# Optimization experiments

Measured on AMD Instinct MI355X. Metric: run time of the kernel, lower is better.

Reference implementation:

```python
import jax, jax.numpy as jnp
import numpy as np

B, P, G, E = 2, 16, 128, 96
C110, C011, C001 = 4, 2, 1
N, CO = 128, 2

def _pw(x, W, b):
    """1x1 conv of any spatial rank == pointwise channel mixing."""
    y = jnp.einsum('oc,bc...->bo...', W, x)
    return y + b.reshape((1, -1) + (1,) * (y.ndim - 2))

def _hidden(s110, s011, s001, Ws, bs):
    # s110:[B,C,P,G,1]  s011:[B,C,1,G,E]  s001:[B,C,1,1,E]
    # sub-stream order: [110 full, 110 pool-P, 110 pool-G, 011 full, 011 pool-G, 011 pool-E, 001]
    t110 = s110[..., 0]         # [B,C,P,G]
    t011 = s011[:, :, 0]        # [B,C,G,E]
    t001 = s001[:, :, 0, 0]     # [B,C,E]
    s = (_pw(t110, Ws[0], bs[0])[..., None]
         + _pw(t110.max(axis=2), Ws[1], bs[1])[:, :, None, :, None]
         + _pw(t110.max(axis=3), Ws[2], bs[2])[:, :, :, None, None]
         + _pw(t011, Ws[3], bs[3])[:, :, None, :, :]
         + _pw(t011.max(axis=2), Ws[4], bs[4])[:, :, None, None, :]
         + _pw(t011.max(axis=3), Ws[5], bs[5])[:, :, None, :, None]
         + _pw(t001, Ws[6], bs[6])[:, :, None, None, :])
    s = jax.nn.leaky_relu(s)    # [B,N,P,G,E]
    return (jnp.max(s, axis=4, keepdims=True),
            jnp.max(s, axis=2, keepdims=True),
            jnp.max(s, axis=(2, 3), keepdims=True))

def _forward(x110, x011, x001, W0_110, b0_110, W0_011, b0_011, W0_001, b0_001, W1, b1, Wact, bact, Wcrit, bcrit):
    Ws0 = [W0_110[0], W0_110[1], W0_110[2], W0_011[0], W0_011[1], W0_011[2], W0_001]
    bs0 = [b0_110[0], b0_110[1], b0_110[2], b0_011[0], b0_011[1], b0_011[2], b0_001]
    s110, s011, s001 = _hidden(x110, x011, x001, Ws0, bs0)
    s110, s011, s001 = _hidden(s110, s011, s001, list(W1), list(b1))
    t110 = s110[..., 0]  # [B,N,P,G]
    # actor head: eliminate G,E via mean pooling (dim_elimination_max_pooling=False)
    a110 = _pw(t110.mean(axis=3), Wact[0], bact[0])              # [B,CO,P]
    a011 = _pw(s011.mean(axis=(3, 4)), Wact[1], bact[1])         # [B,CO,1]
    a001 = _pw(s001[:, :, :, 0].mean(axis=3), Wact[2], bact[2])  # [B,CO,1]
    actions = jax.nn.leaky_relu(a110 + a011 + a001)              # [B,CO,P]
    # critic head: eliminate G via mean pooling
    c110 = _pw(t110.mean(axis=3), Wcrit[0], bcrit[0])            # [B,CO,P]
    c011 = _pw(s011[:, :, 0].mean(axis=2), Wcrit[1], bcrit[1])   # [B,CO,E]
    c001 = _pw(s001[:, :, 0, 0], Wcrit[2], bcrit[2])             # [B,CO,E]
    v = jax.nn.leaky_relu(c110[:, :, :, None] + (c011 + c001)[:, :, None, :])  # [B,CO,P,E]
    v110 = v.max(axis=3).sum(axis=2)  # stream (1,1,0): max over E, sum over P
    v011 = v.max(axis=2).sum(axis=2)  # streams (0,1,1) and (0,0,1) coincide numerically
    values = (2.0 + v110 + 2.0 * v011).reshape(-1)  # python sum(l, 2) starts at 2
    return actions, values

def setup_inputs() -> dict:
    key = jax.random.key(0)
    ks = jax.random.split(key, 12)
    f32 = jnp.float32
    def w(k, shape, fan):
        return jax.random.normal(k, shape, f32) / np.float32(np.sqrt(fan))
    return {
        'x110': jax.random.normal(ks[0], (B, C110, P, G, 1), f32),
        'x011': jax.random.normal(ks[1], (B, C011, 1, G, E), f32),
        'x001': jax.random.normal(ks[2], (B, C001, 1, 1, E), f32),
        'W0_110': w(ks[3], (3, N, C110), C110), 'b0_110': jnp.zeros((3, N), f32),
        'W0_011': w(ks[4], (3, N, C011), C011), 'b0_011': jnp.zeros((3, N), f32),
        'W0_001': w(ks[5], (N, C001), C001),    'b0_001': jnp.zeros((N,), f32),
        'W1':     w(ks[6], (7, N, N), N),       'b1':     jnp.zeros((7, N), f32),
        'Wact':   w(ks[7], (3, CO, N), N),      'bact':   jnp.zeros((3, CO), f32),
        'Wcrit':  w(ks[8], (3, CO, N), N),      'bcrit':  jnp.zeros((3, CO), f32),
    }

def reference(x110, x011, x001, W0_110, b0_110, W0_011, b0_011, W0_001, b0_001, W1, b1, Wact, bact, Wcrit, bcrit):
    return _forward(x110, x011, x001, W0_110, b0_110, W0_011, b0_011, W0_001, b0_001, W1, b1, Wact, bact, Wcrit, bcrit)
```

## Files before the change

kernel.cpp:

```cpp
#include <hip/hip_runtime.h>
#include <math.h>

#define DEVI __device__ __forceinline__

constexpr int B = 2, P = 16, G = 128, E = 96, N = 128, CO = 2;

DEVI float lrelu(float x) { return x > 0.f ? x : 0.01f * x; }

constexpr int OFF_U1     = 0;
constexpr int OFF_V1     = OFF_U1 + 524288;
constexpr int OFF_MAXPU0 = OFF_V1 + 3145728;
constexpr int OFF_MAXEV0 = OFF_MAXPU0 + 32768;
constexpr int OFF_MP110  = OFF_MAXEV0 + 32768;
constexpr int OFF_MG110  = OFF_MP110 + 32768;
constexpr int OFF_S001A  = OFF_MG110 + 4096;
constexpr int OFF_RMP    = OFF_S001A + 24576;
constexpr int OFF_RMG    = OFF_RMP + 1024;
constexpr int OFF_RME    = OFF_RMG + 128;
constexpr int OFF_RMG011 = OFF_RME + 512;
constexpr int OFF_M110   = OFF_RMG011 + 384;
constexpr int OFF_M011E  = OFF_M110 + 4096;
constexpr int OFF_S001B  = OFF_M011E + 24576;
constexpr int OFF_WT     = OFF_S001B + 24576;
constexpr int OFF_PART   = OFF_WT + 81920;

__global__ void __launch_bounds__(256) k_layer0(
    const float* __restrict__ x110, const float* __restrict__ x011,
    const float* __restrict__ x001,
    const float* __restrict__ W0_110, const float* __restrict__ b0_110,
    const float* __restrict__ W0_011, const float* __restrict__ b0_011,
    const float* __restrict__ W0_001, const float* __restrict__ b0_001,
    const float* __restrict__ W1,
    float* __restrict__ maxpU0g, float* __restrict__ maxeV0g,
    float* __restrict__ mp110, float* __restrict__ mg110,
    float* __restrict__ s001a,
    float* __restrict__ rmpG, float* __restrict__ rmgG,
    float* __restrict__ rmeG, float* __restrict__ rmg011G,
    float* __restrict__ wT) {
  __shared__ float xs[4 * 16 * 128];
  __shared__ float v0[128 * 97];
  __shared__ float u0[16 * 128];
  __shared__ float rmp[512], rmgS[64], rme[256], rmg011L[192];
  __shared__ float mpu[128], mev[128], part[256];
  const int bn = blockIdx.x, b = bn >> 7, n = bn & 127, tid = threadIdx.x;

  {
    const float4* xsrc = (const float4*)(x110 + (size_t)b * 8192);
    float4* xdst = (float4*)xs;
#pragma unroll
    for (int k = 0; k < 8; k++) xdst[tid + k * 256] = xsrc[tid + k * 256];
  }
  __syncthreads();
  for (int i = tid; i < 512; i += 256) {
    int c = i >> 7, g = i & 127;
    float m = -INFINITY;
    for (int p = 0; p < P; p++) m = fmaxf(m, xs[(c * 16 + p) * 128 + g]);
    rmp[i] = m;
  }
  if (tid < 64) {
    int c = tid >> 4, p = tid & 15;
    float m = -INFINITY;
    for (int g = 0; g < G; g++) m = fmaxf(m, xs[(c * 16 + p) * 128 + g]);
    rmgS[tid] = m;
  }
  {
    int c = tid >> 7, g = tid & 127;
    const float4* r = (const float4*)(x011 + ((size_t)(b * 2 + c) * 128 + g) * 96);
    float m = -INFINITY;
#pragma unroll
    for (int j = 0; j < 24; j++) {
      float4 v = r[j];
      m = fmaxf(m, fmaxf(fmaxf(v.x, v.y), fmaxf(v.z, v.w)));
    }
    rme[tid] = m;
  }
  if (tid < 192) {
    int c = tid / 96, e = tid % 96;
    const float* pp = x011 + ((size_t)(b * 2 + c) * 128) * 96 + e;
    float m = -INFINITY;
    for (int g = 0; g < G; g++) m = fmaxf(m, pp[g * 96]);
    rmg011L[tid] = m;
  }
  __syncthreads();
  float w0[4], w1[4], w2[4];
#pragma unroll
  for (int cc = 0; cc < 4; cc++) {
    w0[cc] = W0_110[n * 4 + cc];
    w1[cc] = W0_110[512 + n * 4 + cc];
    w2[cc] = W0_110[1024 + n * 4 + cc];
  }
  float we0 = W0_011[512 + n * 2], we1 = W0_011[512 + n * 2 + 1];
  float bu = b0_110[n] + b0_110[128 + n] + b0_110[256 + n] + b0_011[256 + n];
  float vw00 = W0_011[n * 2], vw01 = W0_011[n * 2 + 1];
  float vw10 = W0_011[256 + n * 2], vw11 = W0_011[256 + n * 2 + 1];
  float w001 = W0_001[n];
  float bv = b0_011[n] + b0_011[128 + n] + b0_001[n];

#pragma unroll
  for (int k = 0; k < 8; k++) {
    int i = tid + k * 256, p = i >> 7, g = i & 127;
    float acc = bu + we0 * rme[g] + we1 * rme[128 + g];
#pragma unroll
    for (int cc = 0; cc < 4; cc++)
      acc += w0[cc] * xs[(cc * 16 + p) * 128 + g] + w1[cc] * rmp[cc * 128 + g]
           + w2[cc] * rmgS[cc * 16 + p];
    u0[i] = acc;
  }
  {
    const float* xa = x011 + (size_t)(b * 2) * 12288;
    const float* xb = xa + 12288;
    const float* xc = x001 + b * 96;
    for (int k = 0; k < 48; k++) {
      int i = tid + k * 256;
      int g = i / 96, e = i - g * 96;
      float val = bv + vw00 * xa[i] + vw01 * xb[i]
                + vw10 * rmg011L[e] + vw11 * rmg011L[96 + e] + w001 * xc[e];
      v0[g * 97 + e] = val;
    }
  }
  __syncthreads();
  if (tid < 128) {
    float m = -INFINITY;
    for (int p = 0; p < P; p++) m = fmaxf(m, u0[p * 128 + tid]);
    mpu[tid] = m;
    maxpU0g[bn * 128 + tid] = m;
  }
  {
    int g = tid & 127, h = tid >> 7;
    const float* r = &v0[g * 97 + h * 48];
    float m = -INFINITY;
    for (int j = 0; j < 48; j++) m = fmaxf(m, r[j]);
    part[tid] = m;
  }
  __syncthreads();
  if (tid < 128) {
    float m = fmaxf(part[tid], part[128 + tid]);
    mev[tid] = m;
    maxeV0g[bn * 128 + tid] = m;
    mp110[bn * 128 + tid] = lrelu(mpu[tid] + m);
  }
  __syncthreads();
  {
    int p = tid >> 4, ch = tid & 15;
    float m = -INFINITY;
    for (int g = ch * 8; g < ch * 8 + 8; g++)
      m = fmaxf(m, u0[p * 128 + g] + mev[g]);
    part[tid] = m;
  }
  if (tid < 96) {
    float m = -INFINITY;
    for (int g = 0; g < G; g++) m = fmaxf(m, mpu[g] + v0[g * 97 + tid]);
    s001a[bn * 96 + tid] = lrelu(m);
  }
  __syncthreads();
  if (tid < 16) {
    float m = -INFINITY;
    for (int ch = 0; ch < 16; ch++) m = fmaxf(m, part[tid * 16 + ch]);
    mg110[bn * 16 + tid] = lrelu(m);
  }
  if (n == 0) {
    for (int i = tid; i < 512; i += 256) rmpG[b * 512 + i] = rmp[i];
    if (tid < 64) rmgG[b * 64 + tid] = rmgS[tid];
    rmeG[b * 256 + tid] = rme[tid];
    if (tid < 192) rmg011G[b * 192 + tid] = rmg011L[tid];
  }
  {
    const int gt = bn * 256 + tid;
#pragma unroll
    for (int it = 0; it < 2; it++) {
      int idx = gt + it * 65536;
      if (idx < 81920) {
        int m = idx >> 14, r = idx & 16383;
        int c = r >> 7, nn = r & 127;
        float v;
        if (m == 0)      v = W1[nn * 128 + c];
        else if (m == 1) v = W1[16384 + nn * 128 + c] + W1[5 * 16384 + nn * 128 + c];
        else if (m == 2) v = W1[2 * 16384 + nn * 128 + c];
        else if (m == 3) v = W1[3 * 16384 + nn * 128 + c];
        else             v = W1[4 * 16384 + nn * 128 + c] + W1[6 * 16384 + nn * 128 + c];
        wT[idx] = v;
      }
    }
  }
}

__global__ void __launch_bounds__(512) k_layer1c(
    const float* __restrict__ x110, const float* __restrict__ x011,
    const float* __restrict__ x001,
    const float* __restrict__ W0_110, const float* __restrict__ b0_110,
    const float* __restrict__ W0_011, const float* __restrict__ b0_011,
    const float* __restrict__ W0_001, const float* __restrict__ b0_001,
    const float* __restrict__ maxpU0g, const float* __restrict__ maxeV0g,
    const float* __restrict__ rmpG, const float* __restrict__ rmgG,
    const float* __restrict__ rmeG, const float* __restrict__ rmg011G,
    const float* __restrict__ wT,
    float* __restrict__ U1, float* __restrict__ V1) {
  __shared__ float s110c[128 * 16];
  __shared__ float s011c[128 * 96];
  __shared__ float W0L110[1536], W0L011[768], W0L001[128];
  __shared__ float busum[128], bvsum[128], mpu[128], mev[128];
  __shared__ float x011row[192], rmg011s[192], x001s[96];
  __shared__ float x110col[64], rmg110p[64], rmp4[4], rme2[2];
  const int blk = blockIdx.x;
  const int b = blk >> 7, g = blk & 127;
  const int tid = threadIdx.x;

  for (int i = tid; i < 1536; i += 512) W0L110[i] = W0_110[i];
  for (int i = tid; i < 768; i += 512) W0L011[i] = W0_011[i];
  if (tid < 128) {
    W0L001[tid] = W0_001[tid];
    busum[tid] = b0_110[tid] + b0_110[128 + tid] + b0_110[256 + tid]
               + b0_011[256 + tid];
    bvsum[tid] = b0_011[tid] + b0_011[128 + tid] + b0_001[tid];
    mpu[tid] = maxpU0g[(b * 128 + tid) * 128 + g];
    mev[tid] = maxeV0g[(b * 128 + tid) * 128 + g];
  } else if (tid >= 256 && tid < 448) {
    int i = tid - 256;
    int c = i / 96, e = i % 96;
    x011row[i] = x011[((size_t)(b * 2 + c) * 128 + g) * 96 + e];
    rmg011s[i] = rmg011G[b * 192 + i];
  } else if (tid >= 448 && tid < 512) {
    int i = tid - 448;
    int c = i >> 4, p = i & 15;
    x110col[i] = x110[((size_t)(b * 4 + c) * 16 + p) * 128 + g];
    rmg110p[i] = rmgG[b * 64 + i];
  } else if (tid >= 128 && tid < 224) {
    x001s[tid - 128] = x001[b * 96 + tid - 128];
  } else if (tid >= 224 && tid < 228) {
    rmp4[tid - 224] = rmpG[(b * 4 + tid - 224) * 128 + g];
  } else if (tid >= 228 && tid < 230) {
    rme2[tid - 228] = rmeG[(b * 2 + tid - 228) * 128 + g];
  }
  __syncthreads();

#pragma unroll
  for (int k = 0; k < 4; k++) {
    int i = tid + k * 512, c = i >> 4, p = i & 15;
    float acc = busum[c] + W0L011[512 + c * 2] * rme2[0]
              + W0L011[512 + c * 2 + 1] * rme2[1];
#pragma unroll
    for (int cc = 0; cc < 4; cc++)
      acc += W0L110[c * 4 + cc] * x110col[cc * 16 + p]
           + W0L110[512 + c * 4 + cc] * rmp4[cc]
           + W0L110[1024 + c * 4 + cc] * rmg110p[cc * 16 + p];
    s110c[i] = lrelu(acc + mev[c]);
  }
  for (int k = 0; k < 24; k++) {
    int i = tid + k * 512;
    int c = i / 96, e = i - c * 96;
    float v = bvsum[c]
            + W0L011[c * 2] * x011row[e] + W0L011[c * 2 + 1] * x011row[96 + e]
            + W0L011[256 + c * 2] * rmg011s[e]
            + W0L011[256 + c * 2 + 1] * rmg011s[96 + e]
            + W0L001[c] * x001s[e];
    s011c[i] = lrelu(v + mpu[c]);
  }
  __syncthreads();

  const float* w0T = wT;
  const float* w3T = wT + 3 * 16384;

  {
    int n = tid & 127, ph = tid >> 7;
    float a[4] = {0.f, 0.f, 0.f, 0.f};
    for (int c = 0; c < 128; c++) {
      float w0v = w0T[c * 128 + n];
      float4 s = *(const float4*)&s110c[c * 16 + ph * 4];
      a[0] += w0v * s.x; a[1] += w0v * s.y; a[2] += w0v * s.z; a[3] += w0v * s.w;
    }
    float* dst = U1 + ((size_t)((b * 128 + g) * 16 + ph * 4)) * 128 + n;
#pragma unroll
    for (int j = 0; j < 4; j++) dst[j * 128] = a[j];
  }
  {
    int n0 = (tid >> 3) * 2, e0 = (tid & 7) * 12;
    float4 aA[3], aB[3];
#pragma unroll
    for (int k = 0; k < 3; k++) {
      aA[k] = make_float4(0.f, 0.f, 0.f, 0.f);
      aB[k] = make_float4(0.f, 0.f, 0.f, 0.f);
    }
    for (int c = 0; c < 128; c++) {
      float2 wv = *(const float2*)&w3T[c * 128 + n0];
      float4 s0 = *(const float4*)&s011c[c * 96 + e0];
      float4 s1 = *(const float4*)&s011c[c * 96 + e0 + 4];
      float4 s2 = *(const float4*)&s011c[c * 96 + e0 + 8];
      aA[0].x += wv.x * s0.x; aA[0].y += wv.x * s0.y;
      aA[0].z += wv.x * s0.z; aA[0].w += wv.x * s0.w;
      aA[1].x += wv.x * s1.x; aA[1].y += wv.x * s1.y;
      aA[1].z += wv.x * s1.z; aA[1].w += wv.x * s1.w;
      aA[2].x += wv.x * s2.x; aA[2].y += wv.x * s2.y;
      aA[2].z += wv.x * s2.z; aA[2].w += wv.x * s2.w;
      aB[0].x += wv.y * s0.x; aB[0].y += wv.y * s0.y;
      aB[0].z += wv.y * s0.z; aB[0].w += wv.y * s0.w;
      aB[1].x += wv.y * s1.x; aB[1].y += wv.y * s1.y;
      aB[1].z += wv.y * s1.z; aB[1].w += wv.y * s1.w;
      aB[2].x += wv.y * s2.x; aB[2].y += wv.y * s2.y;
      aB[2].z += wv.y * s2.z; aB[2].w += wv.y * s2.w;
    }
    float* dA = V1 + ((size_t)((b * 128 + g) * 128 + n0)) * 96 + e0;
    float* dB = dA + 96;
#pragma unroll
    for (int k = 0; k < 3; k++) {
      *(float4*)(dA + k * 4) = aA[k];
      *(float4*)(dB + k * 4) = aB[k];
    }
  }
}

__global__ void __launch_bounds__(256) k_post3(
    const float* __restrict__ U1, const float* __restrict__ V1,
    const float* __restrict__ s001a, const float* __restrict__ mp110,
    const float* __restrict__ mg110,
    const float* __restrict__ wT, const float* __restrict__ b1,
    float* __restrict__ partOut) {
  constexpr int GS = 16;
  __shared__ float Vt[GS][8][100];
  __shared__ float Ut[GS][16][9];
  __shared__ float bfL[8][GS];
  __shared__ float egL[8][96];
  __shared__ float cpL[8][16];
  __shared__ float partE[GS][8][4];
  __shared__ float mxeV[GS][8], mxpU[GS][8];
  __shared__ float bbL[8], bvL[8];
  const int blk = blockIdx.x;
  const int b = blk >> 7, nc = (blk >> 3) & 15, gc = blk & 7;
  const int n0 = nc * 8, g0 = gc * 16;
  const int tid = threadIdx.x;
  const float* w15T = wT + 16384;
  const float* w2T  = wT + 2 * 16384;
  const float* w46T = wT + 4 * 16384;

  if (tid < 8) {
    int n = n0 + tid;
    bbL[tid] = b1[n] + b1[128 + n] + b1[256 + n] + b1[640 + n];
    bvL[tid] = b1[384 + n] + b1[512 + n] + b1[768 + n];
  }
  if (tid < 128) {
    int nn = tid >> 4, gl = tid & 15;
    float acc = 0.f;
    for (int c = 0; c < 128; c++)
      acc += w15T[c * 128 + n0 + nn] * mp110[(b * 128 + c) * 128 + g0 + gl];
    bfL[nn][gl] = acc;
  } else {
    int i = tid - 128;
    int nn = i >> 4, p = i & 15;
    float acc = 0.f;
    for (int c = 0; c < 128; c++)
      acc += w2T[c * 128 + n0 + nn] * mg110[(b * 128 + c) * 16 + p];
    cpL[nn][p] = acc;
  }
#pragma unroll
  for (int k = 0; k < 3; k++) {
    int s = tid + k * 256;
    int nn = s / 96, e = s % 96;
    float acc = 0.f;
    for (int c = 0; c < 128; c++)
      acc += w46T[c * 128 + n0 + nn] * s001a[b * 12288 + c * 96 + e];
    egL[nn][e] = acc;
  }
  __syncthreads();

  const size_t Ubase = (size_t)b * 128 * 16 * 128;
  const size_t Vbase = (size_t)b * 128 * 128 * 96;
#pragma unroll
  for (int k = 0; k < 48; k++) {
    int i = tid + k * 256;
    int gs = i / 768, r = i % 768, nn = r / 96, e = r % 96;
    float v = V1[Vbase + ((size_t)(g0 + gs) * 128 + n0 + nn) * 96 + e];
    Vt[gs][nn][e] = v + bvL[nn] + egL[nn][e];
  }
#pragma unroll
  for (int k = 0; k < 8; k++) {
    int i = tid + k * 256;
    int gs = i >> 7, r = i & 127, p = r >> 3, nn = r & 7;
    float u = U1[Ubase + ((size_t)(g0 + gs) * 16 + p) * 128 + n0 + nn];
    Ut[gs][p][nn] = u + bbL[nn] + cpL[nn][p] + bfL[nn][gs];
  }
  __syncthreads();
#pragma unroll
  for (int k = 0; k < 2; k++) {
    int i = tid + k * 256;
    int gs = i >> 5, nn = (i >> 2) & 7, ec = i & 3;
    float m = -INFINITY;
    for (int e = ec * 24; e < ec * 24 + 24; e++) m = fmaxf(m, Vt[gs][nn][e]);
    partE[gs][nn][ec] = m;
  }
  __syncthreads();
  if (tid < 128) {
    int gs = tid >> 3, nn = tid & 7;
    mxeV[gs][nn] = fmaxf(fmaxf(partE[gs][nn][0], partE[gs][nn][1]),
                         fmaxf(partE[gs][nn][2], partE[gs][nn][3]));
    float m = -INFINITY;
    for (int p = 0; p < 16; p++) m = fmaxf(m, Ut[gs][p][nn]);
    mxpU[gs][nn] = m;
  }
  __syncthreads();

  float* pb = partOut + (size_t)blk * 1664;
  if (tid < 128) {
    int nn = tid >> 4, p = tid & 15;
    float a = 0.f;
#pragma unroll
    for (int gs = 0; gs < GS; gs++)
      a += lrelu(Ut[gs][p][nn] + mxeV[gs][nn]);
    pb[tid] = a;
  }
#pragma unroll
  for (int k = 0; k < 3; k++) {
    int s = tid + k * 256;
    int nn = s / 96, e = s % 96;
    float a = 0.f, m = -INFINITY;
#pragma unroll
    for (int gs = 0; gs < GS; gs++) {
      float pre = mxpU[gs][nn] + Vt[gs][nn][e];
      a += lrelu(pre);
      m = fmaxf(m, pre);
    }
    pb[128 + s] = a;
    pb[896 + s] = m;
  }
}

__global__ void __launch_bounds__(256) k_combine(
    const float* __restrict__ partIn,
    float* __restrict__ m110, float* __restrict__ m011e,
    float* __restrict__ s001b) {
  const int blk = blockIdx.x, b = blk >> 4, nc = blk & 15, n0 = nc * 8;
  const int tid = threadIdx.x;
  const float* base = partIn + (size_t)((b * 16 + nc) * 8) * 1664;
  if (tid < 128) {
    int nn = tid >> 4, p = tid & 15;
    float a = 0.f;
#pragma unroll
    for (int gc = 0; gc < 8; gc++) a += base[gc * 1664 + tid];
    m110[(b * 128 + n0 + nn) * 16 + p] = a * (1.f / G);
  }
#pragma unroll
  for (int k = 0; k < 3; k++) {
    int s = tid + k * 256;
    int nn = s / 96, e = s % 96;
    float a = 0.f, m = -INFINITY;
#pragma unroll
    for (int gc = 0; gc < 8; gc++) {
      a += base[gc * 1664 + 128 + s];
      m = fmaxf(m, base[gc * 1664 + 896 + s]);
    }
    m011e[(b * 128 + n0 + nn) * 96 + e] = a * (1.f / G);
    s001b[(b * 128 + n0 + nn) * 96 + e] = lrelu(m);
  }
}

__global__ void __launch_bounds__(128) k_final(const float* __restrict__ m110,
                                               const float* __restrict__ m011e,
                                               const float* __restrict__ s001,
                                               const float* __restrict__ Wact,
                                               const float* __restrict__ bact,
                                               const float* __restrict__ Wcrit,
                                               const float* __restrict__ bcrit,
                                               float* __restrict__ out) {
  __shared__ float buf[128][97];
  __shared__ float m110s[128][17];
  __shared__ float sm011[N], sm001[N], sce1[E], sce[E], scp[P], srow[P], scol[E];
  const int bo = blockIdx.x;
  const int o = bo & 1, b = bo >> 1;
  const int t = threadIdx.x;

#pragma unroll
  for (int k = 0; k < 16; k++) {
    int i = t + k * 128;
    m110s[i >> 4][i & 15] = m110[b * 2048 + i];
  }
  for (int k = 0; k < 96; k++) {
    int i = t + k * 128;
    buf[i / 96][i % 96] = m011e[b * 12288 + i];
  }
  __syncthreads();
  {
    float s = 0.f;
    for (int e = 0; e < E; e++) s += buf[t][e];
    sm011[t] = s * (1.f / E);
  }
  if (t < 96) {
    const float* wc1 = Wcrit + (1 * CO + o) * N;
    float c = 0.f;
    for (int n = 0; n < N; n++) c += wc1[n] * buf[n][t];
    sce1[t] = c;
  }
  __syncthreads();
  for (int k = 0; k < 96; k++) {
    int i = t + k * 128;
    buf[i / 96][i % 96] = s001[b * 12288 + i];
  }
  __syncthreads();
  {
    float s = 0.f;
    for (int e = 0; e < E; e++) s += buf[t][e];
    sm001[t] = s * (1.f / E);
  }
  if (t < 96) {
    const float* wc2 = Wcrit + (2 * CO + o) * N;
    float c = 0.f;
    for (int n = 0; n < N; n++) c += wc2[n] * buf[n][t];
    sce[t] = sce1[t] + c + bcrit[CO + o] + bcrit[2 * CO + o];
  }
  __syncthreads();
  if (t < P) {
    const float* wa0 = Wact + o * N;
    const float* wa1 = Wact + (1 * CO + o) * N;
    const float* wa2 = Wact + (2 * CO + o) * N;
    const float* wc0 = Wcrit + o * N;
    float a = 0.f, c = 0.f, aa = 0.f;
    for (int n = 0; n < N; n++) {
      float m = m110s[n][t];
      a += wa0[n] * m;
      c += wc0[n] * m;
      aa += wa1[n] * sm011[n] + wa2[n] * sm001[n];
    }
    float act = a + aa + bact[o] + bact[CO + o] + bact[2 * CO + o];
    out[(b * CO + o) * P + t] = lrelu(act);
    scp[t] = c + bcrit[o];
  }
  __syncthreads();
  if (t < P) {
    float m = -INFINITY;
    for (int e = 0; e < E; e++) m = fmaxf(m, lrelu(scp[t] + sce[e]));
    srow[t] = m;
  } else if (t < P + E) {
    int e = t - P;
    float m = -INFINITY;
    for (int p = 0; p < P; p++) m = fmaxf(m, lrelu(scp[p] + sce[e]));
    scol[e] = m;
  }
  __syncthreads();
  if (t == 0) {
    float v110 = 0.f, v011 = 0.f;
    for (int p = 0; p < P; p++) v110 += srow[p];
    for (int e = 0; e < E; e++) v011 += scol[e];
    out[B * CO * P + b * CO + o] = 2.f + v110 + 2.f * v011;
  }
}

extern "C" void kernel_launch(void* const* d_in, const int* in_sizes, int n_in,
                              void* d_out, int out_size, void* d_ws, size_t ws_size,
                              hipStream_t stream) {
  const float* x110   = (const float*)d_in[0];
  const float* x011   = (const float*)d_in[1];
  const float* x001   = (const float*)d_in[2];
  const float* W0_110 = (const float*)d_in[3];
  const float* b0_110 = (const float*)d_in[4];
  const float* W0_011 = (const float*)d_in[5];
  const float* b0_011 = (const float*)d_in[6];
  const float* W0_001 = (const float*)d_in[7];
  const float* b0_001 = (const float*)d_in[8];
  const float* W1     = (const float*)d_in[9];
  const float* b1     = (const float*)d_in[10];
  const float* Wact   = (const float*)d_in[11];
  const float* bact   = (const float*)d_in[12];
  const float* Wcrit  = (const float*)d_in[13];
  const float* bcrit  = (const float*)d_in[14];
  float* out = (float*)d_out;
  float* w = (float*)d_ws;

  float* U1     = w + OFF_U1;
  float* V1     = w + OFF_V1;
  float* maxpU0 = w + OFF_MAXPU0;
  float* maxeV0 = w + OFF_MAXEV0;
  float* mp110  = w + OFF_MP110;
  float* mg110  = w + OFF_MG110;
  float* s001a  = w + OFF_S001A;
  float* rmpG   = w + OFF_RMP;
  float* rmgG   = w + OFF_RMG;
  float* rmeG   = w + OFF_RME;
  float* rmg011 = w + OFF_RMG011;
  float* m110   = w + OFF_M110;
  float* m011e  = w + OFF_M011E;
  float* s001b  = w + OFF_S001B;
  float* wT     = w + OFF_WT;
  float* partB  = w + OFF_PART;

  k_layer0<<<256, 256, 0, stream>>>(x110, x011, x001, W0_110, b0_110, W0_011,
                                    b0_011, W0_001, b0_001, W1,
                                    maxpU0, maxeV0, mp110, mg110, s001a,
                                    rmpG, rmgG, rmeG, rmg011, wT);
  k_layer1c<<<256, 512, 0, stream>>>(x110, x011, x001, W0_110, b0_110, W0_011,
                                     b0_011, W0_001, b0_001,
                                     maxpU0, maxeV0, rmpG, rmgG, rmeG, rmg011,
                                     wT, U1, V1);
  k_post3<<<256, 256, 0, stream>>>(U1, V1, s001a, mp110, mg110, wT, b1, partB);
  k_combine<<<32, 256, 0, stream>>>(partB, m110, m011e, s001b);
  k_final<<<4, 128, 0, stream>>>(m110, m011e, s001b, Wact, bact, Wcrit, bcrit, out);
}
```

Measured before the change: 112.6 us.

## Fuse combine into final kernel, halve layer0 LDS, rebalance layer1 GEMM work

Merges k_combine into k_final, which now reduces partB directly with 256 threads, removing one launch and the intermediate m110/m011e/s001b buffers. k_layer0 builds v0 in two 64-row halves to shrink shared memory, allowing more blocks per CU, and reorders the x011 row-max ahead of the first barrier. k_layer1c splits threads so half compute V1 with a 4x12 register tile and half compute U1 with 8 outputs each. k_post3 loads V1 with float4 and pads Vt to 104 for alignment. The fused final kernel runs on only 4 blocks, so the serial reduction tail may grow.

Measured after the change: 119.9 us. 6.5% more time.

```diff
diff --git a/kernel.cpp b/kernel.cpp
--- a/kernel.cpp
+++ b/kernel.cpp
@@ -18,10 +18,7 @@
 constexpr int OFF_RMG    = OFF_RMP + 1024;
 constexpr int OFF_RME    = OFF_RMG + 128;
 constexpr int OFF_RMG011 = OFF_RME + 512;
-constexpr int OFF_M110   = OFF_RMG011 + 384;
-constexpr int OFF_M011E  = OFF_M110 + 4096;
-constexpr int OFF_S001B  = OFF_M011E + 24576;
-constexpr int OFF_WT     = OFF_S001B + 24576;
+constexpr int OFF_WT     = OFF_RMG011 + 384;
 constexpr int OFF_PART   = OFF_WT + 81920;
 
 __global__ void __launch_bounds__(256) k_layer0(
@@ -38,7 +35,7 @@
     float* __restrict__ rmeG, float* __restrict__ rmg011G,
     float* __restrict__ wT) {
   __shared__ float xs[4 * 16 * 128];
-  __shared__ float v0[128 * 97];
+  __shared__ float v0h[64 * 97];
   __shared__ float u0[16 * 128];
   __shared__ float rmp[512], rmgS[64], rme[256], rmg011L[192];
   __shared__ float mpu[128], mev[128], part[256];
@@ -50,19 +47,6 @@
 #pragma unroll
     for (int k = 0; k < 8; k++) xdst[tid + k * 256] = xsrc[tid + k * 256];
   }
-  __syncthreads();
-  for (int i = tid; i < 512; i += 256) {
-    int c = i >> 7, g = i & 127;
-    float m = -INFINITY;
-    for (int p = 0; p < P; p++) m = fmaxf(m, xs[(c * 16 + p) * 128 + g]);
-    rmp[i] = m;
-  }
-  if (tid < 64) {
-    int c = tid >> 4, p = tid & 15;
-    float m = -INFINITY;
-    for (int g = 0; g < G; g++) m = fmaxf(m, xs[(c * 16 + p) * 128 + g]);
-    rmgS[tid] = m;
-  }
   {
     int c = tid >> 7, g = tid & 127;
     const float4* r = (const float4*)(x011 + ((size_t)(b * 2 + c) * 128 + g) * 96);
@@ -73,6 +57,19 @@
       m = fmaxf(m, fmaxf(fmaxf(v.x, v.y), fmaxf(v.z, v.w)));
     }
     rme[tid] = m;
+  }
+  __syncthreads();
+  for (int i = tid; i < 512; i += 256) {
+    int c = i >> 7, g = i & 127;
+    float m = -INFINITY;
+    for (int p = 0; p < P; p++) m = fmaxf(m, xs[(c * 16 + p) * 128 + g]);
+    rmp[i] = m;
+  }
+  if (tid < 64) {
+    int c = tid >> 4, p = tid & 15;
+    float m = -INFINITY;
+    for (int g = 0; g < G; g++) m = fmaxf(m, xs[(c * 16 + p) * 128 + g]);
+    rmgS[tid] = m;
   }
   if (tid < 192) {
     int c = tid / 96, e = tid % 96;
@@ -106,18 +103,6 @@
            + w2[cc] * rmgS[cc * 16 + p];
     u0[i] = acc;
   }
-  {
-    const float* xa = x011 + (size_t)(b * 2) * 12288;
-    const float* xb = xa + 12288;
-    const float* xc = x001 + b * 96;
-    for (int k = 0; k < 48; k++) {
-      int i = tid + k * 256;
-      int g = i / 96, e = i - g * 96;
-      float val = bv + vw00 * xa[i] + vw01 * xb[i]
-                + vw10 * rmg011L[e] + vw11 * rmg011L[96 + e] + w001 * xc[e];
-      v0[g * 97 + e] = val;
-    }
-  }
   __syncthreads();
   if (tid < 128) {
     float m = -INFINITY;
@@ -125,21 +110,45 @@
     mpu[tid] = m;
     maxpU0g[bn * 128 + tid] = m;
   }
-  {
-    int g = tid & 127, h = tid >> 7;
-    const float* r = &v0[g * 97 + h * 48];
-    float m = -INFINITY;
-    for (int j = 0; j < 48; j++) m = fmaxf(m, r[j]);
-    part[tid] = m;
-  }
-  __syncthreads();
-  if (tid < 128) {
-    float m = fmaxf(part[tid], part[128 + tid]);
-    mev[tid] = m;
-    maxeV0g[bn * 128 + tid] = m;
-    mp110[bn * 128 + tid] = lrelu(mpu[tid] + m);
-  }
-  __syncthreads();
+  __syncthreads();
+
+  const float* xa = x011 + (size_t)(b * 2) * 12288;
+  const float* xb = xa + 12288;
+  const float* xc = x001 + b * 96;
+  float runMax = -INFINITY;
+
+  for (int h2 = 0; h2 < 2; h2++) {
+    for (int k = 0; k < 24; k++) {
+      int i = tid + k * 256;
+      int gp = i / 96, e = i - gp * 96;
+      int g = h2 * 64 + gp;
+      float val = bv + vw00 * xa[g * 96 + e] + vw01 * xb[g * 96 + e]
+                + vw10 * rmg011L[e] + vw11 * rmg011L[96 + e] + w001 * xc[e];
+      v0h[gp * 97 + e] = val;
+    }
+    __syncthreads();
+    {
+      int gp = tid & 63, q = tid >> 6;
+      const float* r = &v0h[gp * 97 + q * 24];
+      float m = -INFINITY;
+      for (int j = 0; j < 24; j++) m = fmaxf(m, r[j]);
+      part[q * 64 + gp] = m;
+    }
+    __syncthreads();
+    if (tid < 64) {
+      float m = fmaxf(fmaxf(part[tid], part[64 + tid]),
+                      fmaxf(part[128 + tid], part[192 + tid]));
+      int g = h2 * 64 + tid;
+      mev[g] = m;
+      maxeV0g[bn * 128 + g] = m;
+      mp110[bn * 128 + g] = lrelu(mpu[g] + m);
+    }
+    if (tid < 96) {
+      for (int gp = 0; gp < 64; gp++)
+        runMax = fmaxf(runMax, mpu[h2 * 64 + gp] + v0h[gp * 97 + tid]);
+    }
+    __syncthreads();
+  }
   {
     int p = tid >> 4, ch = tid & 15;
     float m = -INFINITY;
@@ -147,11 +156,7 @@
       m = fmaxf(m, u0[p * 128 + g] + mev[g]);
     part[tid] = m;
   }
-  if (tid < 96) {
-    float m = -INFINITY;
-    for (int g = 0; g < G; g++) m = fmaxf(m, mpu[g] + v0[g * 97 + tid]);
-    s001a[bn * 96 + tid] = lrelu(m);
-  }
+  if (tid < 96) s001a[bn * 96 + tid] = lrelu(runMax);
   __syncthreads();
   if (tid < 16) {
     float m = -INFINITY;
@@ -260,51 +265,51 @@
   const float* w0T = wT;
   const float* w3T = wT + 3 * 16384;
 
-  {
-    int n = tid & 127, ph = tid >> 7;
-    float a[4] = {0.f, 0.f, 0.f, 0.f};
+  if (tid < 256) {
+    int n0 = (tid >> 3) * 4, e0 = (tid & 7) * 12;
+    float4 acc[4][3];
+#pragma unroll
+    for (int ni = 0; ni < 4; ni++)
+#pragma unroll
+      for (int k = 0; k < 3; k++) acc[ni][k] = make_float4(0.f, 0.f, 0.f, 0.f);
     for (int c = 0; c < 128; c++) {
-      float w0v = w0T[c * 128 + n];
-      float4 s = *(const float4*)&s110c[c * 16 + ph * 4];
-      a[0] += w0v * s.x; a[1] += w0v * s.y; a[2] += w0v * s.z; a[3] += w0v * s.w;
-    }
-    float* dst = U1 + ((size_t)((b * 128 + g) * 16 + ph * 4)) * 128 + n;
-#pragma unroll
-    for (int j = 0; j < 4; j++) dst[j * 128] = a[j];
-  }
-  {
-    int n0 = (tid >> 3) * 2, e0 = (tid & 7) * 12;
-    float4 aA[3], aB[3];
-#pragma unroll
-    for (int k = 0; k < 3; k++) {
-      aA[k] = make_float4(0.f, 0.f, 0.f, 0.f);
-      aB[k] = make_float4(0.f, 0.f, 0.f, 0.f);
-    }
-    for (int c = 0; c < 128; c++) {
-      float2 wv = *(const float2*)&w3T[c * 128 + n0];
+      float4 wv = *(const float4*)&w3T[c * 128 + n0];
       float4 s0 = *(const float4*)&s011c[c * 96 + e0];
       float4 s1 = *(const float4*)&s011c[c * 96 + e0 + 4];
       float4 s2 = *(const float4*)&s011c[c * 96 + e0 + 8];
-      aA[0].x += wv.x * s0.x; aA[0].y += wv.x * s0.y;
-      aA[0].z += wv.x * s0.z; aA[0].w += wv.x * s0.w;
-      aA[1].x += wv.x * s1.x; aA[1].y += wv.x * s1.y;
-      aA[1].z += wv.x * s1.z; aA[1].w += wv.x * s1.w;
-      aA[2].x += wv.x * s2.x; aA[2].y += wv.x * s2.y;
-      aA[2].z += wv.x * s2.z; aA[2].w += wv.x * s2.w;
-      aB[0].x += wv.y * s0.x; aB[0].y += wv.y * s0.y;
-      aB[0].z += wv.y * s0.z; aB[0].w += wv.y * s0.w;
-      aB[1].x += wv.y * s1.x; aB[1].y += wv.y * s1.y;
-      aB[1].z += wv.y * s1.z; aB[1].w += wv.y * s1.w;
-      aB[2].x += wv.y * s2.x; aB[2].y += wv.y * s2.y;
-      aB[2].z += wv.y * s2.z; aB[2].w += wv.y * s2.w;
-    }
-    float* dA = V1 + ((size_t)((b * 128 + g) * 128 + n0)) * 96 + e0;
-    float* dB = dA + 96;
-#pragma unroll
-    for (int k = 0; k < 3; k++) {
-      *(float4*)(dA + k * 4) = aA[k];
-      *(float4*)(dB + k * 4) = aB[k];
-    }
+#pragma unroll
+      for (int ni = 0; ni < 4; ni++) {
+        float wc = ni == 0 ? wv.x : ni == 1 ? wv.y : ni == 2 ? wv.z : wv.w;
+        acc[ni][0].x += wc * s0.x; acc[ni][0].y += wc * s0.y;
+        acc[ni][0].z += wc * s0.z; acc[ni][0].w += wc * s0.w;
+        acc[ni][1].x += wc * s1.x; acc[ni][1].y += wc * s1.y;
+        acc[ni][1].z += wc * s1.z; acc[ni][1].w += wc * s1.w;
+        acc[ni][2].x += wc * s2.x; acc[ni][2].y += wc * s2.y;
+        acc[ni][2].z += wc * s2.z; acc[ni][2].w += wc * s2.w;
+      }
+    }
+#pragma unroll
+    for (int ni = 0; ni < 4; ni++) {
+      float* dst = V1 + ((size_t)((b * 128 + g) * 128 + n0 + ni)) * 96 + e0;
+#pragma unroll
+      for (int k = 0; k < 3; k++) *(float4*)(dst + k * 4) = acc[ni][k];
+    }
+  } else {
+    int t = tid - 256;
+    int n = t & 127, ph = t >> 7;
+    float a[8];
+#pragma unroll
+    for (int j = 0; j < 8; j++) a[j] = 0.f;
+    for (int c = 0; c < 128; c++) {
+      float w0v = w0T[c * 128 + n];
+      float4 s0 = *(const float4*)&s110c[c * 16 + ph * 8];
+      float4 s1 = *(const float4*)&s110c[c * 16 + ph * 8 + 4];
+      a[0] += w0v * s0.x; a[1] += w0v * s0.y; a[2] += w0v * s0.z; a[3] += w0v * s0.w;
+      a[4] += w0v * s1.x; a[5] += w0v * s1.y; a[6] += w0v * s1.z; a[7] += w0v * s1.w;
+    }
+    float* dst = U1 + ((size_t)((b * 128 + g) * 16 + ph * 8)) * 128 + n;
+#pragma unroll
+    for (int j = 0; j < 8; j++) dst[j * 128] = a[j];
   }
 }
 
@@ -315,7 +320,7 @@
     const float* __restrict__ wT, const float* __restrict__ b1,
     float* __restrict__ partOut) {
   constexpr int GS = 16;
-  __shared__ float Vt[GS][8][100];
+  __shared__ float Vt[GS][8][104];
   __shared__ float Ut[GS][16][9];
   __shared__ float bfL[8][GS];
   __shared__ float egL[8][96];
@@ -364,11 +369,16 @@
   const size_t Ubase = (size_t)b * 128 * 16 * 128;
   const size_t Vbase = (size_t)b * 128 * 128 * 96;
 #pragma unroll
-  for (int k = 0; k < 48; k++) {
-    int i = tid + k * 256;
-    int gs = i / 768, r = i % 768, nn = r / 96, e = r % 96;
-    float v = V1[Vbase + ((size_t)(g0 + gs) * 128 + n0 + nn) * 96 + e];
-    Vt[gs][nn][e] = v + bvL[nn] + egL[nn][e];
+  for (int k = 0; k < 12; k++) {
+    int i4 = tid + k * 256;
+    int gs = i4 / 192, r = i4 % 192, nn = r / 24, e4 = r % 24;
+    float4 v = *(const float4*)(V1 + Vbase
+                 + ((size_t)(g0 + gs) * 128 + n0 + nn) * 96 + e4 * 4);
+    float bvv = bvL[nn];
+    const float* eg = &egL[nn][e4 * 4];
+    float4 o = make_float4(v.x + bvv + eg[0], v.y + bvv + eg[1],
+                           v.z + bvv + eg[2], v.w + bvv + eg[3]);
+    *(float4*)&Vt[gs][nn][e4 * 4] = o;
   }
 #pragma unroll
   for (int k = 0; k < 8; k++) {
@@ -422,61 +432,41 @@
   }
 }
 
-__global__ void __launch_bounds__(256) k_combine(
+__global__ void __launch_bounds__(256) k_final(
     const float* __restrict__ partIn,
-    float* __restrict__ m110, float* __restrict__ m011e,
-    float* __restrict__ s001b) {
-  const int blk = blockIdx.x, b = blk >> 4, nc = blk & 15, n0 = nc * 8;
-  const int tid = threadIdx.x;
-  const float* base = partIn + (size_t)((b * 16 + nc) * 8) * 1664;
-  if (tid < 128) {
-    int nn = tid >> 4, p = tid & 15;
-    float a = 0.f;
-#pragma unroll
-    for (int gc = 0; gc < 8; gc++) a += base[gc * 1664 + tid];
-    m110[(b * 128 + n0 + nn) * 16 + p] = a * (1.f / G);
-  }
-#pragma unroll
-  for (int k = 0; k < 3; k++) {
-    int s = tid + k * 256;
-    int nn = s / 96, e = s % 96;
-    float a = 0.f, m = -INFINITY;
-#pragma unroll
-    for (int gc = 0; gc < 8; gc++) {
-      a += base[gc * 1664 + 128 + s];
-      m = fmaxf(m, base[gc * 1664 + 896 + s]);
-    }
-    m011e[(b * 128 + n0 + nn) * 96 + e] = a * (1.f / G);
-    s001b[(b * 128 + n0 + nn) * 96 + e] = lrelu(m);
-  }
-}
-
-__global__ void __launch_bounds__(128) k_final(const float* __restrict__ m110,
-                                               const float* __restrict__ m011e,
-                                               const float* __restrict__ s001,
-                                               const float* __restrict__ Wact,
-                                               const float* __restrict__ bact,
-                                               const float* __restrict__ Wcrit,
-                                               const float* __restrict__ bcrit,
-                                               float* __restrict__ out) {
+    const float* __restrict__ Wact, const float* __restrict__ bact,
+    const float* __restrict__ Wcrit, const float* __restrict__ bcrit,
+    float* __restrict__ out) {
   __shared__ float buf[128][97];
   __shared__ float m110s[128][17];
   __shared__ float sm011[N], sm001[N], sce1[E], sce[E], scp[P], srow[P], scol[E];
   const int bo = blockIdx.x;
   const int o = bo & 1, b = bo >> 1;
   const int t = threadIdx.x;
-
-#pragma unroll
-  for (int k = 0; k < 16; k++) {
-    int i = t + k * 128;
-    m110s[i >> 4][i & 15] = m110[b * 2048 + i];
-  }
-  for (int k = 0; k < 96; k++) {
-    int i = t + k * 128;
-    buf[i / 96][i % 96] = m011e[b * 12288 + i];
-  }
-  __syncthreads();
-  {
+  const float* pbB = partIn + (size_t)(b * 16) * 8 * 1664;
+
+#pragma unroll
+  for (int k = 0; k < 8; k++) {
+    int i = t + k * 256;
+    int nc = i >> 7, j = i & 127;
+    const float* base = pbB + (size_t)(nc * 8) * 1664;
+    float a = 0.f;
+#pragma unroll
+    for (int gc = 0; gc < 8; gc++) a += base[gc * 1664 + j];
+    m110s[nc * 8 + (j >> 4)][j & 15] = a * (1.f / G);
+  }
+#pragma unroll
+  for (int k = 0; k < 48; k++) {
+    int i = t + k * 256;
+    int nc = i / 768, r = i % 768;
+    const float* base = pbB + (size_t)(nc * 8) * 1664;
+    float a = 0.f;
+#pragma unroll
+    for (int gc = 0; gc < 8; gc++) a += base[gc * 1664 + 128 + r];
+    buf[nc * 8 + r / 96][r % 96] = a * (1.f / G);
+  }
+  __syncthreads();
+  if (t < 128) {
     float s = 0.f;
     for (int e = 0; e < E; e++) s += buf[t][e];
     sm011[t] = s * (1.f / E);
@@ -488,12 +478,18 @@
     sce1[t] = c;
   }
   __syncthreads();
-  for (int k = 0; k < 96; k++) {
-    int i = t + k * 128;
-    buf[i / 96][i % 96] = s001[b * 12288 + i];
-  }
-  __syncthreads();
-  {
+#pragma unroll
+  for (int k = 0; k < 48; k++) {
+    int i = t + k * 256;
+    int nc = i / 768, r = i % 768;
+    const float* base = pbB + (size_t)(nc * 8) * 1664;
+    float m = -INFINITY;
+#pragma unroll
+    for (int gc = 0; gc < 8; gc++) m = fmaxf(m, base[gc * 1664 + 896 + r]);
+    buf[nc * 8 + r / 96][r % 96] = lrelu(m);
+  }
+  __syncthreads();
+  if (t < 128) {
     float s = 0.f;
     for (int e = 0; e < E; e++) s += buf[t][e];
     sm001[t] = s * (1.f / E);
@@ -573,9 +569,6 @@
   float* rmgG   = w + OFF_RMG;
   float* rmeG   = w + OFF_RME;
   float* rmg011 = w + OFF_RMG011;
-  float* m110   = w + OFF_M110;
-  float* m011e  = w + OFF_M011E;
-  float* s001b  = w + OFF_S001B;
   float* wT     = w + OFF_WT;
   float* partB  = w + OFF_PART;
 
@@ -588,6 +581,5 @@
                                      maxpU0, maxeV0, rmpG, rmgG, rmeG, rmg011,
                                      wT, U1, V1);
   k_post3<<<256, 256, 0, stream>>>(U1, V1, s001a, mp110, mg110, wT, b1, partB);
-  k_combine<<<32, 256, 0, stream>>>(partB, m110, m011e, s001b);
-  k_final<<<4, 128, 0, stream>>>(m110, m011e, s001b, Wact, bact, Wcrit, bcrit, out);
+  k_final<<<4, 256, 0, stream>>>(partB, Wact, bact, Wcrit, bcrit, out);
 }
```
